# Kernel tuning notes

Hardware: AMD Instinct MI355X
Metric: run time of the kernel (lower is better)

## Reference

```python
import jax, jax.numpy as jnp
import numpy as np

B, N, C = 16, 1024, 768
H = 12
HD = C // H
MLP = 4 * C
EPS = 1e-5  # torch nn.LayerNorm default
LS_INIT = 1e-5


def _ln(x, g, b):
    mu = jnp.mean(x, axis=-1, keepdims=True)
    var = jnp.var(x, axis=-1, keepdims=True)
    return (x - mu) * jax.lax.rsqrt(var + EPS) * g + b


def setup_inputs() -> dict:
    key = jax.random.key(0)
    ks = jax.random.split(key, 8)
    s = 0.02
    return {
        "x": jax.random.normal(ks[0], (B, N, C), dtype=jnp.float32),
        "w_qkv": jax.random.normal(ks[1], (C, 3 * C), dtype=jnp.float32) * s,
        "w_proj": jax.random.normal(ks[2], (C, C), dtype=jnp.float32) * s,
        "b_proj": jnp.zeros((C,), jnp.float32),
        "ln1_g": jnp.ones((C,), jnp.float32),
        "ln1_b": jnp.zeros((C,), jnp.float32),
        "ln2_g": jnp.ones((C,), jnp.float32),
        "ln2_b": jnp.zeros((C,), jnp.float32),
        "ls1_g": jnp.full((C,), LS_INIT, jnp.float32),
        "ls2_g": jnp.full((C,), LS_INIT, jnp.float32),
        "w_fc1": jax.random.normal(ks[3], (C, MLP), dtype=jnp.float32) * s,
        "b_fc1": jnp.zeros((MLP,), jnp.float32),
        "w_fc2": jax.random.normal(ks[4], (MLP, C), dtype=jnp.float32) * s,
        "b_fc2": jnp.zeros((C,), jnp.float32),
    }


def reference(x, w_qkv, w_proj, b_proj, ln1_g, ln1_b, ln2_g, ln2_b,
              ls1_g, ls2_g, w_fc1, b_fc1, w_fc2, b_fc2):
    scale = HD ** -0.5
    # ---- attention branch (pre-norm) ----
    h = x
    y = _ln(x, ln1_g, ln1_b)
    qkv = (y @ w_qkv).reshape(B, N, 3, H, HD)
    q, k, v = (jnp.moveaxis(qkv, 2, 0)[i].transpose(0, 2, 1, 3) for i in range(3))  # [B,H,N,HD]
    attn = jnp.einsum("bhnd,bhmd->bhnm", q * scale, k)
    attn = attn - jnp.max(attn, axis=-1, keepdims=True)  # explicit max-subtract as in source
    attn = jax.nn.softmax(attn, axis=-1)
    o = jnp.einsum("bhnm,bhmd->bhnd", attn, v).transpose(0, 2, 1, 3).reshape(B, N, C)
    o = o @ w_proj + b_proj
    x = h + o * ls1_g  # LayerScale (fp32)
    # ---- MLP branch ----
    h = x
    y = _ln(x, ln2_g, ln2_b)
    y = jax.nn.gelu(y @ w_fc1 + b_fc1, approximate=False)
    y = y @ w_fc2 + b_fc2
    x = h + y * ls2_g
    return x  # weights=None since vis=False
```

## Files before the change

### kernel.cpp

```cpp
#include <hip/hip_runtime.h>
#include <cstdint>
#include <cstddef>

typedef __bf16 bf16;
typedef __bf16 bf16x4 __attribute__((ext_vector_type(4)));
typedef __bf16 bf16x8 __attribute__((ext_vector_type(8)));
typedef _Float16 f16;
typedef _Float16 f16x4 __attribute__((ext_vector_type(4)));
typedef _Float16 f16x8 __attribute__((ext_vector_type(8)));
typedef float  f32x4  __attribute__((ext_vector_type(4)));
typedef unsigned char u8;

#define B_   16
#define N_   1024
#define C_   768
#define H_   12
#define HD_  64
#define M_   (B_*N_)
#define MLP_ 3072
#define QKVN 2304
#define WSCALE 64.0f
#define WINV  (1.0f/64.0f)

__device__ __forceinline__ void gll16(const void* g, void* l) {
  __builtin_amdgcn_global_load_lds((const __attribute__((address_space(1))) void*)g,
                                   (__attribute__((address_space(3))) void*)l,
                                   16, 0, 0);
}

__device__ __forceinline__ float fast_exp2(float x) {
  return __builtin_amdgcn_exp2f(x);
}

__device__ __forceinline__ u8 to_fp8(float a) {
  return (u8)(__builtin_amdgcn_cvt_pk_fp8_f32(a, a, 0, false) & 0xff);
}
__device__ __forceinline__ int to_fp8x4(float v0, float v1, float v2, float v3) {
  int p = __builtin_amdgcn_cvt_pk_fp8_f32(v0, v1, 0, false);
  p = __builtin_amdgcn_cvt_pk_fp8_f32(v2, v3, p, true);
  return p;
}

__device__ __forceinline__ float fast_gelu(float t) {
  float z = 2.30220568f * (t + 0.044715f * t * t * t);
  return t / (1.0f + fast_exp2(-z));
}

__global__ void transpose_cast(const float* __restrict__ w, u8* __restrict__ wt,
                               int K, int N) {
  __shared__ float tile[32][33];
  int n0 = blockIdx.x * 32, k0 = blockIdx.y * 32;
  int tx = threadIdx.x, ty = threadIdx.y;
  #pragma unroll
  for (int i = 0; i < 32; i += 8)
    tile[ty + i][tx] = w[(size_t)(k0 + ty + i) * N + n0 + tx];
  __syncthreads();
  #pragma unroll
  for (int i = 0; i < 32; i += 8)
    wt[(size_t)(n0 + ty + i) * K + k0 + tx] = to_fp8(tile[tx][ty + i] * WSCALE);
}

__global__ __launch_bounds__(256)
void ln_cast_kernel(const float* __restrict__ x, const float* __restrict__ g,
                    const float* __restrict__ bta, u8* __restrict__ y) {
  int row = blockIdx.x;
  int tid = threadIdx.x;
  const float* xr = x + (size_t)row * C_;
  float v0 = xr[tid], v1 = xr[tid + 256], v2 = xr[tid + 512];
  float s  = v0 + v1 + v2;
  float sq = v0 * v0 + v1 * v1 + v2 * v2;
  #pragma unroll
  for (int off = 32; off > 0; off >>= 1) {
    s  += __shfl_xor(s,  off);
    sq += __shfl_xor(sq, off);
  }
  __shared__ float red[8];
  int wave = tid >> 6, lane = tid & 63;
  if (lane == 0) { red[wave] = s; red[4 + wave] = sq; }
  __syncthreads();
  s  = red[0] + red[1] + red[2] + red[3];
  sq = red[4] + red[5] + red[6] + red[7];
  float mean = s * (1.0f / C_);
  float var  = sq * (1.0f / C_) - mean * mean;
  float rstd = rsqrtf(var + 1e-5f);
  u8* yr = y + (size_t)row * C_;
  yr[tid]       = to_fp8((v0 - mean) * rstd * g[tid]       + bta[tid]);
  yr[tid + 256] = to_fp8((v1 - mean) * rstd * g[tid + 256] + bta[tid + 256]);
  yr[tid + 512] = to_fp8((v2 - mean) * rstd * g[tid + 512] + bta[tid + 512]);
}

template <int EPI>
__global__ __launch_bounds__(256)
void gemm_bt(const u8* __restrict__ A, const u8* __restrict__ Bt,
             void* __restrict__ outp, const float* __restrict__ bias,
             const float* __restrict__ ls, const float* __restrict__ resid,
             int M, int N, int K, int nb) {
  constexpr int BM = 128, BN = 128, BK = 64;
  __shared__ __align__(16) u8 As[BM * BK];
  __shared__ __align__(16) u8 Bs[BN * BK];
  int tid  = threadIdx.x;
  int lane = tid & 63, wave = tid >> 6;
  int quad = lane >> 4, l16 = lane & 15;
  int bid = blockIdx.x;
  int xcd = bid & 7, seq = bid >> 3;
  int mi = xcd + 8 * (seq / nb), ni = seq % nb;
  int m0 = mi * BM, n0 = ni * BN;
  int wm = (wave >> 1) * 64, wn = (wave & 1) * 64;

  const u8* ag[2]; const u8* bg[2];
  #pragma unroll
  for (int s = 0; s < 2; s++) {
    int u = tid + s * 256;
    int r = u >> 2, g = (u & 3) ^ ((r >> 1) & 3);
    ag[s] = A  + (size_t)(m0 + r) * K + g * 16;
    bg[s] = Bt + (size_t)(n0 + r) * K + g * 16;
  }
  int swz = (l16 >> 1) & 3;

  const f32x4 fz = {0.f, 0.f, 0.f, 0.f};
  f32x4 acc[4][4];
  #pragma unroll
  for (int i = 0; i < 4; i++)
    #pragma unroll
    for (int j = 0; j < 4; j++) acc[i][j] = fz;

  for (int k0 = 0; k0 < K; k0 += BK) {
    gll16(ag[0] + k0, As + tid * 16);
    gll16(ag[1] + k0, As + 4096 + tid * 16);
    gll16(bg[0] + k0, Bs + tid * 16);
    gll16(bg[1] + k0, Bs + 4096 + tid * 16);
    __syncthreads();
    long af[4][2], bfr[4][2];
    #pragma unroll
    for (int i = 0; i < 4; i++)
      #pragma unroll
      for (int kk = 0; kk < 2; kk++)
        af[i][kk] = *(const long*)(As + (wm + i * 16 + l16) * 64
                                   + (((kk << 1) | (quad >> 1)) ^ swz) * 16 + (quad & 1) * 8);
    #pragma unroll
    for (int j = 0; j < 4; j++)
      #pragma unroll
      for (int kk = 0; kk < 2; kk++)
        bfr[j][kk] = *(const long*)(Bs + (wn + j * 16 + l16) * 64
                                    + (((kk << 1) | (quad >> 1)) ^ swz) * 16 + (quad & 1) * 8);
    #pragma unroll
    for (int kk = 0; kk < 2; kk++)
      #pragma unroll
      for (int i = 0; i < 4; i++)
        #pragma unroll
        for (int j = 0; j < 4; j++)
          acc[i][j] = __builtin_amdgcn_mfma_f32_16x16x32_fp8_fp8(af[i][kk], bfr[j][kk],
                                                                 acc[i][j], 0, 0, 0);
    __syncthreads();
  }

  #pragma unroll
  for (int i = 0; i < 4; i++) {
    int rowb = m0 + wm + i * 16 + quad * 4;
    #pragma unroll
    for (int j = 0; j < 4; j++) {
      int col = n0 + wn + j * 16 + l16;
      #pragma unroll
      for (int r = 0; r < 4; r++) {
        float v = acc[i][j][r] * WINV;
        size_t idx = (size_t)(rowb + r) * N + col;
        if constexpr (EPI == 0) {
          ((bf16*)outp)[idx] = (bf16)v;
        } else if constexpr (EPI == 1) {
          ((float*)outp)[idx] = resid[idx] + (v + bias[col]) * ls[col];
        } else if constexpr (EPI == 2) {
          ((u8*)outp)[idx] = to_fp8(fast_gelu(v + bias[col]));
        } else {
          ((float*)outp)[idx] = resid[idx] + (v + bias[col]) * ls[col];
        }
      }
    }
  }
}

__global__ void transpose_v(const bf16* __restrict__ qkv, f16* __restrict__ vt) {
  __shared__ bf16 tile[32][33];
  int bh = blockIdx.z;
  int b = bh / H_, h = bh % H_;
  int n0 = blockIdx.x * 32, d0 = blockIdx.y * 32;
  int tx = threadIdx.x, ty = threadIdx.y;
  const bf16* src = qkv + (size_t)(b * N_) * QKVN + 2 * C_ + h * HD_;
  #pragma unroll
  for (int i = 0; i < 32; i += 8)
    tile[ty + i][tx] = src[(size_t)(n0 + ty + i) * QKVN + d0 + tx];
  __syncthreads();
  f16* dst = vt + (size_t)bh * HD_ * N_;
  #pragma unroll
  for (int i = 0; i < 32; i += 8)
    dst[(size_t)(d0 + ty + i) * N_ + n0 + tx] = (f16)(float)tile[tx][ty + i];
}

__global__ __launch_bounds__(256)
void attn_kernel(const bf16* __restrict__ qkv, const f16* __restrict__ vt,
                 u8* __restrict__ o) {
  constexpr int KSTR = 72;
  constexpr int VSTR = 136;
  __shared__ __align__(16) bf16 Ks[128 * KSTR];
  __shared__ __align__(16) f16  Vs[HD_ * VSTR];

  int tid = threadIdx.x, lane = tid & 63, wave = tid >> 6;
  int quad = lane >> 4, l16 = lane & 15;
  int bid = blockIdx.x;
  int xcd = bid & 7, seq = bid >> 3;
  int bh = xcd + 8 * (seq >> 3);
  int b = bh / H_, h = bh % H_;
  int q0 = (seq & 7) * 128;
  const float CEXP = 0.125f * 1.44269504f;

  bf16x8 qf[2][2];
  #pragma unroll
  for (int i = 0; i < 2; i++)
    #pragma unroll
    for (int kk = 0; kk < 2; kk++)
      qf[i][kk] = *(const bf16x8*)(qkv + (size_t)(b * N_ + q0 + wave * 32 + i * 16 + l16) * QKVN
                                   + h * HD_ + kk * 32 + quad * 8);

  const f32x4 fz = {0.f, 0.f, 0.f, 0.f};
  f32x4 oacc[2][4];
  float m_run[2], l_run[2];
  #pragma unroll
  for (int i = 0; i < 2; i++) {
    #pragma unroll
    for (int jd = 0; jd < 4; jd++) oacc[i][jd] = fz;
    m_run[i] = -1e30f; l_run[i] = 0.f;
  }

  const bf16* kbase = qkv + (size_t)(b * N_) * QKVN + C_ + h * HD_;
  const f16*  vbase = vt + (size_t)bh * HD_ * N_;

  int kr[4], kc[4], vr[4], vc[4];
  #pragma unroll
  for (int u = 0; u < 4; u++) {
    int L = tid + u * 256;
    kr[u] = L >> 3;  kc[u] = (L & 7) * 8;
    vr[u] = L >> 4;  vc[u] = (L & 15) * 8;
  }

  bf16x8 kreg[4]; f16x8 vreg[4];
  #pragma unroll
  for (int u = 0; u < 4; u++) {
    kreg[u] = *(const bf16x8*)(kbase + (size_t)kr[u] * QKVN + kc[u]);
    vreg[u] = *(const f16x8*)(vbase + (size_t)vr[u] * N_ + vc[u]);
  }

  for (int kv = 0; kv < N_; kv += 128) {
    __syncthreads();
    #pragma unroll
    for (int u = 0; u < 4; u++) {
      *(bf16x8*)(Ks + kr[u] * KSTR + kc[u]) = kreg[u];
      *(f16x8*)(Vs + vr[u] * VSTR + vc[u])  = vreg[u];
    }
    __syncthreads();

    if (kv + 128 < N_) {
      #pragma unroll
      for (int u = 0; u < 4; u++) {
        kreg[u] = *(const bf16x8*)(kbase + (size_t)(kv + 128 + kr[u]) * QKVN + kc[u]);
        vreg[u] = *(const f16x8*)(vbase + (size_t)vr[u] * N_ + kv + 128 + vc[u]);
      }
    }

    f32x4 sv[2][8];
    #pragma unroll
    for (int i = 0; i < 2; i++)
      #pragma unroll
      for (int kf = 0; kf < 8; kf++) sv[i][kf] = fz;
    #pragma unroll
    for (int kk = 0; kk < 2; kk++) {
      #pragma unroll
      for (int kf = 0; kf < 8; kf++) {
        bf16x8 kb = *(const bf16x8*)(Ks + (kf * 16 + l16) * KSTR + kk * 32 + quad * 8);
        sv[0][kf] = __builtin_amdgcn_mfma_f32_16x16x32_bf16(kb, qf[0][kk], sv[0][kf], 0, 0, 0);
        sv[1][kf] = __builtin_amdgcn_mfma_f32_16x16x32_bf16(kb, qf[1][kk], sv[1][kf], 0, 0, 0);
      }
    }

    f16x4 pb[2][8];
    #pragma unroll
    for (int i = 0; i < 2; i++) {
      float mx = sv[i][0][0];
      #pragma unroll
      for (int kf = 0; kf < 8; kf++)
        #pragma unroll
        for (int r = 0; r < 4; r++) mx = fmaxf(mx, sv[i][kf][r]);
      mx = fmaxf(mx, __shfl_xor(mx, 16));
      mx = fmaxf(mx, __shfl_xor(mx, 32));
      float mold = m_run[i];
      float mnew = fmaxf(mold, mx);
      float mb   = mnew * CEXP;
      float al   = fast_exp2(mold * CEXP - mb);
      float rs = 0.f;
      #pragma unroll
      for (int kf = 0; kf < 8; kf++) {
        #pragma unroll
        for (int r = 0; r < 4; r++) {
          float p = fast_exp2(sv[i][kf][r] * CEXP - mb);
          pb[i][kf][r] = (f16)p;
          rs += p;
        }
      }
      rs += __shfl_xor(rs, 16);
      rs += __shfl_xor(rs, 32);
      m_run[i] = mnew;
      l_run[i] = l_run[i] * al + rs;
      #pragma unroll
      for (int jd = 0; jd < 4; jd++) oacc[i][jd] *= al;
    }

    #pragma unroll
    for (int kc2 = 0; kc2 < 8; kc2++) {
      #pragma unroll
      for (int jd = 0; jd < 4; jd++) {
        f16x4 va = *(const f16x4*)(Vs + (jd * 16 + l16) * VSTR + kc2 * 16 + quad * 4);
        oacc[0][jd] = __builtin_amdgcn_mfma_f32_16x16x16f16(va, pb[0][kc2], oacc[0][jd], 0, 0, 0);
        oacc[1][jd] = __builtin_amdgcn_mfma_f32_16x16x16f16(va, pb[1][kc2], oacc[1][jd], 0, 0, 0);
      }
    }
  }

  #pragma unroll
  for (int i = 0; i < 2; i++) {
    float inv = 1.0f / l_run[i];
    int n = q0 + wave * 32 + i * 16 + l16;
    #pragma unroll
    for (int jd = 0; jd < 4; jd++) {
      int p = to_fp8x4(oacc[i][jd][0] * inv, oacc[i][jd][1] * inv,
                       oacc[i][jd][2] * inv, oacc[i][jd][3] * inv);
      *(int*)(o + (size_t)(b * N_ + n) * C_ + h * HD_ + jd * 16 + quad * 4) = p;
    }
  }
}

#define WQKVT_OFF  0u
#define WPROJT_OFF 1769472u
#define WFC1T_OFF  2359296u
#define WFC2T_OFF  4718592u
#define Y_OFF      7077888u
#define QKV_OFF    19660800u
#define VT_OFF     95158272u
#define O_OFF      120324096u
#define X1_OFF     132907008u
#define WS_NEEDED  183238656u

extern "C" void kernel_launch(void* const* d_in, const int* in_sizes, int n_in,
                              void* d_out, int out_size, void* d_ws, size_t ws_size,
                              hipStream_t stream) {
  if (ws_size < (size_t)WS_NEEDED) return;

  const float* x      = (const float*)d_in[0];
  const float* w_qkv  = (const float*)d_in[1];
  const float* w_proj = (const float*)d_in[2];
  const float* b_proj = (const float*)d_in[3];
  const float* ln1_g  = (const float*)d_in[4];
  const float* ln1_b  = (const float*)d_in[5];
  const float* ln2_g  = (const float*)d_in[6];
  const float* ln2_b  = (const float*)d_in[7];
  const float* ls1_g  = (const float*)d_in[8];
  const float* ls2_g  = (const float*)d_in[9];
  const float* w_fc1  = (const float*)d_in[10];
  const float* b_fc1  = (const float*)d_in[11];
  const float* w_fc2  = (const float*)d_in[12];
  const float* b_fc2  = (const float*)d_in[13];

  char* ws = (char*)d_ws;
  u8*    wqkvT  = (u8*)(ws + WQKVT_OFF);
  u8*    wprojT = (u8*)(ws + WPROJT_OFF);
  u8*    wfc1T  = (u8*)(ws + WFC1T_OFF);
  u8*    wfc2T  = (u8*)(ws + WFC2T_OFF);
  u8*    y      = (u8*)(ws + Y_OFF);
  bf16*  qkv    = (bf16*)(ws + QKV_OFF);
  u8*    hbuf   = (u8*)(ws + QKV_OFF);
  f16*   vt     = (f16*)(ws + VT_OFF);
  u8*    o      = (u8*)(ws + O_OFF);
  float* x1     = (float*)(ws + X1_OFF);
  float* out    = (float*)d_out;

  dim3 tb(32, 8);
  transpose_cast<<<dim3(QKVN / 32, C_ / 32), tb, 0, stream>>>(w_qkv,  wqkvT,  C_,   QKVN);
  transpose_cast<<<dim3(C_   / 32, C_ / 32), tb, 0, stream>>>(w_proj, wprojT, C_,   C_);
  transpose_cast<<<dim3(MLP_ / 32, C_ / 32), tb, 0, stream>>>(w_fc1,  wfc1T,  C_,   MLP_);
  transpose_cast<<<dim3(C_ / 32, MLP_ / 32), tb, 0, stream>>>(w_fc2,  wfc2T,  MLP_, C_);

  ln_cast_kernel<<<M_, 256, 0, stream>>>(x, ln1_g, ln1_b, y);

  gemm_bt<0><<<(QKVN / 128) * 128, 256, 0, stream>>>(
      y, wqkvT, qkv, nullptr, nullptr, nullptr, M_, QKVN, C_, QKVN / 128);

  transpose_v<<<dim3(N_ / 32, HD_ / 32, B_ * H_), tb, 0, stream>>>(qkv, vt);

  attn_kernel<<<(N_ / 128) * B_ * H_, 256, 0, stream>>>(qkv, vt, o);

  gemm_bt<1><<<(C_ / 128) * 128, 256, 0, stream>>>(
      o, wprojT, x1, b_proj, ls1_g, x, M_, C_, C_, C_ / 128);

  ln_cast_kernel<<<M_, 256, 0, stream>>>(x1, ln2_g, ln2_b, y);

  gemm_bt<2><<<(MLP_ / 128) * 128, 256, 0, stream>>>(
      y, wfc1T, hbuf, b_fc1, nullptr, nullptr, M_, MLP_, C_, MLP_ / 128);

  gemm_bt<3><<<(C_ / 128) * 128, 256, 0, stream>>>(
      hbuf, wfc2T, out, b_fc2, ls2_g, x1, M_, C_, MLP_, C_ / 128);
}
```

Before: 549.8 us.

## Replace direct global-to-LDS loads with register-prefetched software pipelining in GEMM

The GEMM main loop no longer uses global_load_lds. It now prefetches the next K-tile into registers while MFMAs run on the current tile held in LDS, then writes that tile to swizzled LDS at the top of the next iteration. The swizzle moves from the global address to the LDS write address. Launch bounds now ask for 4 blocks per CU, which adds register pressure and can cause spills, and each iteration still has two barriers.

```diff
diff --git a/kernel.cpp b/kernel.cpp
--- a/kernel.cpp
+++ b/kernel.cpp
@@ -21,12 +21,6 @@
 #define QKVN 2304
 #define WSCALE 64.0f
 #define WINV  (1.0f/64.0f)
-
-__device__ __forceinline__ void gll16(const void* g, void* l) {
-  __builtin_amdgcn_global_load_lds((const __attribute__((address_space(1))) void*)g,
-                                   (__attribute__((address_space(3))) void*)l,
-                                   16, 0, 0);
-}
 
 __device__ __forceinline__ float fast_exp2(float x) {
   return __builtin_amdgcn_exp2f(x);
@@ -90,7 +84,7 @@
 }
 
 template <int EPI>
-__global__ __launch_bounds__(256)
+__global__ __launch_bounds__(256, 4)
 void gemm_bt(const u8* __restrict__ A, const u8* __restrict__ Bt,
              void* __restrict__ outp, const float* __restrict__ bias,
              const float* __restrict__ ls, const float* __restrict__ resid,
@@ -107,13 +101,15 @@
   int m0 = mi * BM, n0 = ni * BN;
   int wm = (wave >> 1) * 64, wn = (wave & 1) * 64;
 
-  const u8* ag[2]; const u8* bg[2];
+  const u8* ag[2]; const u8* bg[2]; u8* asw[2]; u8* bsw[2];
   #pragma unroll
   for (int s = 0; s < 2; s++) {
     int u = tid + s * 256;
-    int r = u >> 2, g = (u & 3) ^ ((r >> 1) & 3);
-    ag[s] = A  + (size_t)(m0 + r) * K + g * 16;
-    bg[s] = Bt + (size_t)(n0 + r) * K + g * 16;
+    int r = u >> 2, g = u & 3, gs = g ^ ((r >> 1) & 3);
+    ag[s]  = A  + (size_t)(m0 + r) * K + g * 16;
+    bg[s]  = Bt + (size_t)(n0 + r) * K + g * 16;
+    asw[s] = As + r * 64 + gs * 16;
+    bsw[s] = Bs + r * 64 + gs * 16;
   }
   int swz = (l16 >> 1) & 3;
 
@@ -124,34 +120,47 @@
     #pragma unroll
     for (int j = 0; j < 4; j++) acc[i][j] = fz;
 
+  int4 apre[2], bpre[2];
+  #pragma unroll
+  for (int s = 0; s < 2; s++) {
+    apre[s] = *(const int4*)ag[s];
+    bpre[s] = *(const int4*)bg[s];
+  }
+
   for (int k0 = 0; k0 < K; k0 += BK) {
-    gll16(ag[0] + k0, As + tid * 16);
-    gll16(ag[1] + k0, As + 4096 + tid * 16);
-    gll16(bg[0] + k0, Bs + tid * 16);
-    gll16(bg[1] + k0, Bs + 4096 + tid * 16);
     __syncthreads();
-    long af[4][2], bfr[4][2];
-    #pragma unroll
-    for (int i = 0; i < 4; i++)
-      #pragma unroll
-      for (int kk = 0; kk < 2; kk++)
-        af[i][kk] = *(const long*)(As + (wm + i * 16 + l16) * 64
-                                   + (((kk << 1) | (quad >> 1)) ^ swz) * 16 + (quad & 1) * 8);
-    #pragma unroll
-    for (int j = 0; j < 4; j++)
-      #pragma unroll
-      for (int kk = 0; kk < 2; kk++)
-        bfr[j][kk] = *(const long*)(Bs + (wn + j * 16 + l16) * 64
-                                    + (((kk << 1) | (quad >> 1)) ^ swz) * 16 + (quad & 1) * 8);
-    #pragma unroll
-    for (int kk = 0; kk < 2; kk++)
+    #pragma unroll
+    for (int s = 0; s < 2; s++) {
+      *(int4*)asw[s] = apre[s];
+      *(int4*)bsw[s] = bpre[s];
+    }
+    __syncthreads();
+
+    if (k0 + BK < K) {
+      #pragma unroll
+      for (int s = 0; s < 2; s++) {
+        apre[s] = *(const int4*)(ag[s] + k0 + BK);
+        bpre[s] = *(const int4*)(bg[s] + k0 + BK);
+      }
+    }
+
+    #pragma unroll
+    for (int kk = 0; kk < 2; kk++) {
+      int go = (((kk << 1) | (quad >> 1)) ^ swz) * 16 + (quad & 1) * 8;
+      long af[4], bfr[4];
+      #pragma unroll
+      for (int i = 0; i < 4; i++)
+        af[i] = *(const long*)(As + (wm + i * 16 + l16) * 64 + go);
+      #pragma unroll
+      for (int j = 0; j < 4; j++)
+        bfr[j] = *(const long*)(Bs + (wn + j * 16 + l16) * 64 + go);
       #pragma unroll
       for (int i = 0; i < 4; i++)
         #pragma unroll
         for (int j = 0; j < 4; j++)
-          acc[i][j] = __builtin_amdgcn_mfma_f32_16x16x32_fp8_fp8(af[i][kk], bfr[j][kk],
+          acc[i][j] = __builtin_amdgcn_mfma_f32_16x16x32_fp8_fp8(af[i], bfr[j],
                                                                  acc[i][j], 0, 0, 0);
-    __syncthreads();
+    }
   }
 
   #pragma unroll
```

Measured after the change: 811.5 us. 47.6% more time.

## Double-buffer LDS tiles in FP8 GEMM to overlap loads with MFMA

Applied to the files above, without the earlier changes.

The GEMM kernel now keeps two LDS buffers for the A and B tiles. It prefetches the first K-tile before the loop, and inside the loop it issues the async global-to-LDS loads for the next tile into the other buffer before running the MFMAs on the current one. This removes the second barrier per iteration and lets memory traffic run alongside compute. In exchange it doubles LDS use per block, which may lower occupancy, and correctness relies on the barrier draining the outstanding loads.

```diff
diff --git a/kernel.cpp b/kernel.cpp
--- a/kernel.cpp
+++ b/kernel.cpp
@@ -96,8 +96,8 @@
              const float* __restrict__ ls, const float* __restrict__ resid,
              int M, int N, int K, int nb) {
   constexpr int BM = 128, BN = 128, BK = 64;
-  __shared__ __align__(16) u8 As[BM * BK];
-  __shared__ __align__(16) u8 Bs[BN * BK];
+  __shared__ __align__(16) u8 As[2][BM * BK];
+  __shared__ __align__(16) u8 Bs[2][BM * BK];
   int tid  = threadIdx.x;
   int lane = tid & 63, wave = tid >> 6;
   int quad = lane >> 4, l16 = lane & 15;
@@ -124,34 +124,38 @@
     #pragma unroll
     for (int j = 0; j < 4; j++) acc[i][j] = fz;
 
+  gll16(ag[0], &As[0][0] + tid * 16);
+  gll16(ag[1], &As[0][0] + 4096 + tid * 16);
+  gll16(bg[0], &Bs[0][0] + tid * 16);
+  gll16(bg[1], &Bs[0][0] + 4096 + tid * 16);
+
+  int buf = 0;
   for (int k0 = 0; k0 < K; k0 += BK) {
-    gll16(ag[0] + k0, As + tid * 16);
-    gll16(ag[1] + k0, As + 4096 + tid * 16);
-    gll16(bg[0] + k0, Bs + tid * 16);
-    gll16(bg[1] + k0, Bs + 4096 + tid * 16);
     __syncthreads();
-    long af[4][2], bfr[4][2];
-    #pragma unroll
-    for (int i = 0; i < 4; i++)
-      #pragma unroll
-      for (int kk = 0; kk < 2; kk++)
-        af[i][kk] = *(const long*)(As + (wm + i * 16 + l16) * 64
-                                   + (((kk << 1) | (quad >> 1)) ^ swz) * 16 + (quad & 1) * 8);
-    #pragma unroll
-    for (int j = 0; j < 4; j++)
-      #pragma unroll
-      for (int kk = 0; kk < 2; kk++)
-        bfr[j][kk] = *(const long*)(Bs + (wn + j * 16 + l16) * 64
-                                    + (((kk << 1) | (quad >> 1)) ^ swz) * 16 + (quad & 1) * 8);
-    #pragma unroll
-    for (int kk = 0; kk < 2; kk++)
+    if (k0 + BK < K) {
+      gll16(ag[0] + k0 + BK, &As[buf ^ 1][0] + tid * 16);
+      gll16(ag[1] + k0 + BK, &As[buf ^ 1][0] + 4096 + tid * 16);
+      gll16(bg[0] + k0 + BK, &Bs[buf ^ 1][0] + tid * 16);
+      gll16(bg[1] + k0 + BK, &Bs[buf ^ 1][0] + 4096 + tid * 16);
+    }
+    #pragma unroll
+    for (int kk = 0; kk < 2; kk++) {
+      int go = (((kk << 1) | (quad >> 1)) ^ swz) * 16 + (quad & 1) * 8;
+      long af[4], bfr[4];
+      #pragma unroll
+      for (int i = 0; i < 4; i++)
+        af[i] = *(const long*)(&As[buf][0] + (wm + i * 16 + l16) * 64 + go);
+      #pragma unroll
+      for (int j = 0; j < 4; j++)
+        bfr[j] = *(const long*)(&Bs[buf][0] + (wn + j * 16 + l16) * 64 + go);
       #pragma unroll
       for (int i = 0; i < 4; i++)
         #pragma unroll
         for (int j = 0; j < 4; j++)
-          acc[i][j] = __builtin_amdgcn_mfma_f32_16x16x32_fp8_fp8(af[i][kk], bfr[j][kk],
+          acc[i][j] = __builtin_amdgcn_mfma_f32_16x16x32_fp8_fp8(af[i], bfr[j],
                                                                  acc[i][j], 0, 0, 0);
-    __syncthreads();
+    }
+    buf ^= 1;
   }
 
   #pragma unroll
```

New measurement: 535.2 us. 1.03x faster.
